# Optimization experiments

Hardware: AMD Instinct MI355X
Metric: run time of the kernel (lower is better)

The kernel has to match this reference:

```python
import jax, jax.numpy as jnp
import numpy as np

B, C, HH, WW = 8, 512, 32, 32
HEADS, GROUPS, EPS = 8, 32, 1e-5


def setup_inputs() -> dict:
    key = jax.random.key(0)
    k0, k1, k2 = jax.random.split(key, 3)
    x = jax.random.normal(k0, (B, C, HH, WW), jnp.float32)
    gamma = jnp.ones((C,), jnp.float32)
    beta = jnp.zeros((C,), jnp.float32)
    # 1x1 convs modeled as (out, in) matrices; fan-in scaling keeps logits sane
    w_qkv = jax.random.normal(k1, (3 * C, C), jnp.float32) * (C ** -0.5)
    b_qkv = jnp.zeros((3 * C,), jnp.float32)
    w_proj = jax.random.normal(k2, (C, C), jnp.float32) * (C ** -0.5)
    b_proj = jnp.zeros((C,), jnp.float32)
    return {"x": x, "gamma": gamma, "beta": beta, "w_qkv": w_qkv,
            "b_qkv": b_qkv, "w_proj": w_proj, "b_proj": b_proj}


def reference(x, gamma, beta, w_qkv, b_qkv, w_proj, b_proj):
    b, c, h, w = x.shape
    S = h * w
    xr = x.reshape(b, c, S)
    # GroupNorm(32, C) over (channels_in_group, spatial)
    xg = xr.reshape(b, GROUPS, c // GROUPS, S)
    mu = xg.mean(axis=(2, 3), keepdims=True)
    var = xg.var(axis=(2, 3), keepdims=True)
    xn = ((xg - mu) * jax.lax.rsqrt(var + EPS)).reshape(b, c, S)
    xn = xn * gamma[None, :, None] + beta[None, :, None]
    # qkv 1x1 conv: (B, 3C, S)
    qkv = jnp.einsum('oc,bcs->bos', w_qkv, xn) + b_qkv[None, :, None]
    D = c // HEADS
    qkv = qkv.reshape(b, 3, HEADS, D, S)  # channel layout: (three, H, D)
    q = jnp.transpose(qkv[:, 0], (0, 1, 3, 2))  # (B, H, S, D)
    k = jnp.transpose(qkv[:, 1], (0, 1, 3, 2))
    v = jnp.transpose(qkv[:, 2], (0, 1, 3, 2))
    scale = 1.0 / float(np.sqrt(np.sqrt(D)))
    logits = jnp.einsum('bhtd,bhsd->bhts', q * scale, k * scale)  # (B,H,S,S)
    logits = logits - jnp.max(logits, axis=-1, keepdims=True)
    probs = jax.nn.softmax(logits, axis=-1)  # dropout p=0 (default)
    attn = jnp.einsum('bhts,bhsd->bhtd', probs, v)  # (B,H,S,D)
    hout = jnp.transpose(attn, (0, 1, 3, 2)).reshape(b, c, S)  # (B, H*D=C, S)
    hout = jnp.einsum('oc,bcs->bos', w_proj, hout) + b_proj[None, :, None]
    return (hout + xr).reshape(b, c, h, w)
```

## Files before the change

### kernel.cpp

```cpp
#include <hip/hip_runtime.h>
#include <hip/hip_bf16.h>

typedef __hip_bfloat16 bf16;
typedef unsigned short u16;
typedef __attribute__((ext_vector_type(8))) short bf16x8;
typedef __attribute__((ext_vector_type(16))) float f32x16;

static constexpr int Bn = 8;
static constexpr int C = 512;
static constexpr int S = 1024;
static constexpr int NH = 8;
static constexpr int HD = 64;
static constexpr int CPG = 16;
#define EPSV 1e-5f
#define QSCALE 0.18033688011112042f

__device__ __forceinline__ u16 f2bf(float f) {
    bf16 h = __float2bfloat16(f);
    return *reinterpret_cast<u16*>(&h);
}
__device__ __forceinline__ unsigned pack_bf2(float a, float b) {
    __hip_bfloat162 h = __float22bfloat162_rn(make_float2(a, b));
    return *reinterpret_cast<unsigned*>(&h);
}

__device__ __forceinline__ void plswap32(unsigned a, unsigned b, unsigned& x, unsigned& y) {
    typedef __attribute__((ext_vector_type(2))) int v2i;
    v2i r = __builtin_amdgcn_permlane32_swap((int)a, (int)b, false, false);
    x = (unsigned)r[0];
    y = (unsigned)r[1];
}

__device__ __forceinline__ void async_copy16(const void* g, void* l) {
    __builtin_amdgcn_global_load_lds(
        (const __attribute__((address_space(1))) void*)g,
        (__attribute__((address_space(3))) void*)l, 16, 0, 0);
}

__global__ __launch_bounds__(256) void prep(const float* __restrict__ x,
                                            const float* __restrict__ wqkv,
                                            const float* __restrict__ wproj,
                                            const float* __restrict__ gamma,
                                            const float* __restrict__ beta,
                                            u16* __restrict__ wbf,
                                            u16* __restrict__ xnt) {
    const int tid = threadIdx.x;
    __shared__ float xs[CPG * S];
    if (blockIdx.x < 256) {
        const int bg = blockIdx.x;
        const int b = bg >> 5, g = bg & 31;
        const size_t base = (size_t)bg * CPG * S;
        const int N = CPG * S;
        float sum = 0.f, sq = 0.f;
        for (int i = tid * 4; i < N; i += 1024) {
            float4 v = *reinterpret_cast<const float4*>(&x[base + i]);
            sum += v.x + v.y + v.z + v.w;
            sq += v.x * v.x + v.y * v.y + v.z * v.z + v.w * v.w;
            *reinterpret_cast<float4*>(&xs[i]) = v;
        }
#pragma unroll
        for (int off = 32; off > 0; off >>= 1) {
            sum += __shfl_down(sum, off, 64);
            sq  += __shfl_down(sq,  off, 64);
        }
        __shared__ float s0[4], s1[4];
        __shared__ float sgb[32];
        __shared__ float smu, srstd;
        if ((tid & 63) == 0) { s0[tid >> 6] = sum; s1[tid >> 6] = sq; }
        if (tid < 16) {
            sgb[tid] = gamma[g * CPG + tid];
            sgb[16 + tid] = beta[g * CPG + tid];
        }
        __syncthreads();
        if (tid == 0) {
            float a  = s0[0] + s0[1] + s0[2] + s0[3];
            float b2 = s1[0] + s1[1] + s1[2] + s1[3];
            float mu = a / (float)N;
            float var = fmaxf(b2 / (float)N - mu * mu, 0.f);
            smu = mu;
            srstd = rsqrtf(var + EPSV);
        }
        __syncthreads();
        const float mu = smu, rstd = srstd;
#pragma unroll
        for (int it = 0; it < 8; ++it) {
            int idx = it * 256 + tid;
            int s = idx >> 1, jh = idx & 1;
            u16 t8[8];
#pragma unroll
            for (int j = 0; j < 8; ++j) {
                int c = jh * 8 + j;
                float v = (xs[c * S + s] - mu) * rstd;
                t8[j] = f2bf(v * sgb[c] + sgb[16 + c]);
            }
            *reinterpret_cast<uint4*>(&xnt[(size_t)(b * S + s) * C + g * CPG + jh * 8]) =
                *reinterpret_cast<uint4*>(t8);
        }
    } else {
        int idx = (blockIdx.x - 256) * 1024 + tid * 4;
        float4 v;
        float sc = 1.f;
        if (idx < 1536 * 512) {
            v = *reinterpret_cast<const float4*>(&wqkv[idx]);
            if (idx < 512 * 512) sc = QSCALE;
        } else {
            v = *reinterpret_cast<const float4*>(&wproj[idx - 1536 * 512]);
        }
        u16 t[4] = {f2bf(v.x * sc), f2bf(v.y * sc), f2bf(v.z * sc), f2bf(v.w * sc)};
        *reinterpret_cast<uint2*>(&wbf[idx]) = *reinterpret_cast<uint2*>(t);
    }
}

__global__ __launch_bounds__(256) void qkv_gemm(const u16* __restrict__ Wb,
                                                const u16* __restrict__ Xt,
                                                const float* __restrict__ bias,
                                                u16* __restrict__ qkvT,
                                                u16* __restrict__ qkvV) {
    const int K = 512;
    const int b = blockIdx.z, o0 = blockIdx.y * 128, s0 = blockIdx.x * 128;
    const int tid = threadIdx.x;
    const int lane = tid & 63, w = tid >> 6;
    const int l31 = lane & 31, half = lane >> 5;
    const int wr = w >> 1, wc = w & 1;
    __shared__ u16 As[128 * 64];
    __shared__ u16 Bs[128 * 64];
    f32x16 acc[2][2] = {};
    const u16* Xb = Xt + (size_t)(b * S + s0) * K;
    for (int k0 = 0; k0 < K; k0 += 64) {
#pragma unroll
        for (int i = 0; i < 4; ++i) {
            int ci = w * 4 + i;
            int r = ci * 8 + (lane >> 3);
            int c = (lane & 7) ^ (r & 7);
            async_copy16(&Wb[(size_t)(o0 + r) * K + k0 + c * 8], &As[ci * 512]);
            async_copy16(&Xb[(size_t)r * K + k0 + c * 8], &Bs[ci * 512]);
        }
        __syncthreads();
#pragma unroll
        for (int kk = 0; kk < 4; ++kk) {
            int c8 = kk * 2 + half;
            bf16x8 af[2], bfr[2];
#pragma unroll
            for (int mt = 0; mt < 2; ++mt) {
                int R = wr * 64 + mt * 32 + l31;
                af[mt] = *reinterpret_cast<const bf16x8*>(
                    &As[R * 64 + ((c8 ^ (R & 7)) << 3)]);
            }
#pragma unroll
            for (int nt = 0; nt < 2; ++nt) {
                int R = wc * 64 + nt * 32 + l31;
                bfr[nt] = *reinterpret_cast<const bf16x8*>(
                    &Bs[R * 64 + ((c8 ^ (R & 7)) << 3)]);
            }
#pragma unroll
            for (int mt = 0; mt < 2; ++mt)
#pragma unroll
                for (int nt = 0; nt < 2; ++nt)
                    acc[mt][nt] = __builtin_amdgcn_mfma_f32_32x32x16_bf16(
                        af[mt], bfr[nt], acc[mt][nt], 0, 0, 0);
        }
        __syncthreads();
    }
    if (o0 < 1024) {
        float bsc = (o0 < 512) ? QSCALE : 1.f;
#pragma unroll
        for (int mt = 0; mt < 2; ++mt) {
#pragma unroll
            for (int g = 0; g < 4; ++g) {
                int o_b = o0 + wr * 64 + mt * 32 + g * 8 + half * 4;
                float4 bz = *reinterpret_cast<const float4*>(&bias[o_b]);
#pragma unroll
                for (int nt = 0; nt < 2; ++nt) {
                    int s = s0 + wc * 64 + nt * 32 + l31;
                    uint2 pk;
                    pk.x = pack_bf2(acc[mt][nt][g * 4 + 0] + bz.x * bsc,
                                    acc[mt][nt][g * 4 + 1] + bz.y * bsc);
                    pk.y = pack_bf2(acc[mt][nt][g * 4 + 2] + bz.z * bsc,
                                    acc[mt][nt][g * 4 + 3] + bz.w * bsc);
                    *reinterpret_cast<uint2*>(&qkvT[(size_t)(b * S + s) * 1024 + o_b]) = pk;
                }
            }
        }
    } else {
#pragma unroll
        for (int mt = 0; mt < 2; ++mt) {
#pragma unroll
            for (int g = 0; g < 4; ++g) {
                int o_b = o0 - 1024 + wr * 64 + mt * 32 + g * 8 + half * 4;
                float4 bz = *reinterpret_cast<const float4*>(&bias[1024 + o_b]);
                float bza[4] = {bz.x, bz.y, bz.z, bz.w};
#pragma unroll
                for (int nt = 0; nt < 2; ++nt) {
                    int s = s0 + wc * 64 + nt * 32 + l31;
#pragma unroll
                    for (int r = 0; r < 4; ++r)
                        qkvV[(size_t)(b * 512 + o_b + r) * S + s] =
                            f2bf(acc[mt][nt][g * 4 + r] + bza[r]);
                }
            }
        }
    }
}

__global__ __launch_bounds__(256) void proj_gemm(const u16* __restrict__ Wb,
                                                 const u16* __restrict__ Xt,
                                                 const float* __restrict__ bias,
                                                 const float* __restrict__ resid,
                                                 float* __restrict__ Yf) {
    const int K = 512;
    const int b = blockIdx.z, o0 = blockIdx.y * 64, s0 = blockIdx.x * 128;
    const int tid = threadIdx.x;
    const int lane = tid & 63, w = tid >> 6;
    const int l31 = lane & 31, half = lane >> 5;
    const int wr = w >> 1, wc = w & 1;
    __shared__ u16 As[64 * 64];
    __shared__ u16 Bs[128 * 64];
    f32x16 acc[2] = {};
    const u16* Xb = Xt + (size_t)(b * S + s0) * K;
    for (int k0 = 0; k0 < K; k0 += 64) {
#pragma unroll
        for (int i = 0; i < 2; ++i) {
            int ci = w * 2 + i;
            int r = ci * 8 + (lane >> 3);
            int c = (lane & 7) ^ (r & 7);
            async_copy16(&Wb[(size_t)(o0 + r) * K + k0 + c * 8], &As[ci * 512]);
        }
#pragma unroll
        for (int i = 0; i < 4; ++i) {
            int ci = w * 4 + i;
            int r = ci * 8 + (lane >> 3);
            int c = (lane & 7) ^ (r & 7);
            async_copy16(&Xb[(size_t)r * K + k0 + c * 8], &Bs[ci * 512]);
        }
        __syncthreads();
#pragma unroll
        for (int kk = 0; kk < 4; ++kk) {
            int c8 = kk * 2 + half;
            int Ra = wr * 32 + l31;
            bf16x8 af = *reinterpret_cast<const bf16x8*>(
                &As[Ra * 64 + ((c8 ^ (Ra & 7)) << 3)]);
#pragma unroll
            for (int nt = 0; nt < 2; ++nt) {
                int R = wc * 64 + nt * 32 + l31;
                bf16x8 bfr = *reinterpret_cast<const bf16x8*>(
                    &Bs[R * 64 + ((c8 ^ (R & 7)) << 3)]);
                acc[nt] = __builtin_amdgcn_mfma_f32_32x32x16_bf16(
                    af, bfr, acc[nt], 0, 0, 0);
            }
        }
        __syncthreads();
    }
#pragma unroll
    for (int g = 0; g < 4; ++g) {
        int o_b = o0 + wr * 32 + g * 8 + half * 4;
        float4 bz = *reinterpret_cast<const float4*>(&bias[o_b]);
        float bza[4] = {bz.x, bz.y, bz.z, bz.w};
#pragma unroll
        for (int nt = 0; nt < 2; ++nt) {
            int s = s0 + wc * 64 + nt * 32 + l31;
#pragma unroll
            for (int r = 0; r < 4; ++r) {
                size_t idx = (size_t)(b * C + o_b + r) * S + s;
                Yf[idx] = acc[nt][g * 4 + r] + bza[r] + resid[idx];
            }
        }
    }
}

__global__ __launch_bounds__(256) void attn_mfma(const u16* __restrict__ qkvT,
                                                 const u16* __restrict__ qkvV,
                                                 u16* __restrict__ houtt) {
    const int b = blockIdx.x >> 3, h = blockIdx.x & 7, q0 = blockIdx.y * 128;
    const int tid = threadIdx.x;
    const int lane = tid & 63, w = tid >> 6;
    const int l31 = lane & 31, half = lane >> 5;
    __shared__ u16 ks[2][64 * 64];
    __shared__ u16 vs[2][64 * 64];

    const u16* qrow = qkvT + (size_t)(b * S + q0 + w * 32 + l31) * 1024 + h * HD;
    const u16* krow = qkvT + (size_t)b * S * 1024 + 512 + h * HD;
    const u16* vrow = qkvV + (size_t)(b * 512 + h * HD) * S;

    bf16x8 qfrag[4];
#pragma unroll
    for (int kk = 0; kk < 4; ++kk)
        qfrag[kk] = *reinterpret_cast<const bf16x8*>(&qrow[kk * 16 + half * 8]);

#pragma unroll
    for (int i = 0; i < 2; ++i) {
        int ci = w * 2 + i;
        int r = ci * 8 + (lane >> 3);
        int c = (lane & 7) ^ (r & 7);
        async_copy16(&krow[(size_t)r * 1024 + c * 8], &ks[0][ci * 512]);
        async_copy16(&vrow[(size_t)r * S + c * 8], &vs[0][ci * 512]);
    }
    __syncthreads();

    f32x16 o_acc[2] = {};
    float l_i = 0.f;

    for (int t = 0; t < 16; ++t) {
        const int cur = t & 1, nxt = cur ^ 1;
        if (t < 15) {
            int kt = (t + 1) * 64;
#pragma unroll
            for (int i = 0; i < 2; ++i) {
                int ci = w * 2 + i;
                int r = ci * 8 + (lane >> 3);
                int c = (lane & 7) ^ (r & 7);
                async_copy16(&krow[(size_t)(kt + r) * 1024 + c * 8], &ks[nxt][ci * 512]);
                async_copy16(&vrow[(size_t)r * S + kt + c * 8], &vs[nxt][ci * 512]);
            }
        }
        f32x16 s_acc[2] = {};
        __builtin_amdgcn_s_setprio(1);
#pragma unroll
        for (int mt = 0; mt < 2; ++mt) {
            int r = mt * 32 + l31;
#pragma unroll
            for (int kk = 0; kk < 4; ++kk) {
                int c8 = kk * 2 + half;
                bf16x8 kf = *reinterpret_cast<const bf16x8*>(
                    &ks[cur][r * 64 + ((c8 ^ (r & 7)) << 3)]);
                s_acc[mt] = __builtin_amdgcn_mfma_f32_32x32x16_bf16(
                    kf, qfrag[kk], s_acc[mt], 0, 0, 0);
            }
        }
        __builtin_amdgcn_s_setprio(0);
        float rsp0 = 0.f, rsp1 = 0.f, rsp2 = 0.f, rsp3 = 0.f;
#pragma unroll
        for (int mt = 0; mt < 2; ++mt)
#pragma unroll
            for (int g = 0; g < 4; ++g) {
                float p0 = __builtin_amdgcn_exp2f(s_acc[mt][g * 4 + 0]);
                float p1 = __builtin_amdgcn_exp2f(s_acc[mt][g * 4 + 1]);
                float p2 = __builtin_amdgcn_exp2f(s_acc[mt][g * 4 + 2]);
                float p3 = __builtin_amdgcn_exp2f(s_acc[mt][g * 4 + 3]);
                s_acc[mt][g * 4 + 0] = p0;
                s_acc[mt][g * 4 + 1] = p1;
                s_acc[mt][g * 4 + 2] = p2;
                s_acc[mt][g * 4 + 3] = p3;
                rsp0 += p0; rsp1 += p1; rsp2 += p2; rsp3 += p3;
            }
        l_i += (rsp0 + rsp1) + (rsp2 + rsp3);
        bf16x8 pf[4];
#pragma unroll
        for (int mt = 0; mt < 2; ++mt)
#pragma unroll
            for (int gp = 0; gp < 2; ++gp) {
                unsigned a_lo = pack_bf2(s_acc[mt][gp * 8 + 0], s_acc[mt][gp * 8 + 1]);
                unsigned a_hi = pack_bf2(s_acc[mt][gp * 8 + 2], s_acc[mt][gp * 8 + 3]);
                unsigned b_lo = pack_bf2(s_acc[mt][gp * 8 + 4], s_acc[mt][gp * 8 + 5]);
                unsigned b_hi = pack_bf2(s_acc[mt][gp * 8 + 6], s_acc[mt][gp * 8 + 7]);
                unsigned u0, u1, u2, u3;
                plswap32(a_lo, b_lo, u0, u2);
                plswap32(a_hi, b_hi, u1, u3);
                union { unsigned u[4]; bf16x8 v; } wv;
                wv.u[0] = u0; wv.u[1] = u1; wv.u[2] = u2; wv.u[3] = u3;
                pf[mt * 2 + gp] = wv.v;
            }
        __builtin_amdgcn_s_setprio(1);
#pragma unroll
        for (int nt = 0; nt < 2; ++nt) {
            int rv = nt * 32 + l31;
#pragma unroll
            for (int kk = 0; kk < 4; ++kk) {
                int c8 = kk * 2 + half;
                bf16x8 vf = *reinterpret_cast<const bf16x8*>(
                    &vs[cur][rv * 64 + ((c8 ^ (rv & 7)) << 3)]);
                o_acc[nt] = __builtin_amdgcn_mfma_f32_32x32x16_bf16(
                    vf, pf[kk], o_acc[nt], 0, 0, 0);
            }
        }
        __builtin_amdgcn_s_setprio(0);
        __syncthreads();
    }
    l_i += __shfl_xor(l_i, 32, 64);
    float inv = 1.f / l_i;
    u16* orow = houtt + (size_t)(b * S + q0 + w * 32 + l31) * 512 + h * HD;
#pragma unroll
    for (int nt = 0; nt < 2; ++nt)
#pragma unroll
        for (int g = 0; g < 4; ++g) {
            uint2 pk;
            pk.x = pack_bf2(o_acc[nt][g * 4 + 0] * inv, o_acc[nt][g * 4 + 1] * inv);
            pk.y = pack_bf2(o_acc[nt][g * 4 + 2] * inv, o_acc[nt][g * 4 + 3] * inv);
            *reinterpret_cast<uint2*>(&orow[nt * 32 + g * 8 + half * 4]) = pk;
        }
}

extern "C" void kernel_launch(void* const* d_in, const int* in_sizes, int n_in,
                              void* d_out, int out_size, void* d_ws, size_t ws_size,
                              hipStream_t stream) {
    const float* x      = (const float*)d_in[0];
    const float* gamma  = (const float*)d_in[1];
    const float* beta   = (const float*)d_in[2];
    const float* w_qkv  = (const float*)d_in[3];
    const float* b_qkv  = (const float*)d_in[4];
    const float* w_proj = (const float*)d_in[5];
    const float* b_proj = (const float*)d_in[6];
    float* out = (float*)d_out;

    char* ws = (char*)d_ws;
    u16* wbf   = (u16*)ws;
    u16* xnt   = (u16*)(ws + 2097152);
    u16* qkvT  = (u16*)(ws + 2097152 + 8388608);
    u16* qkvV  = (u16*)(ws + 2097152 + 8388608 + 16777216);
    u16* houtt = xnt;

    prep<<<1280, 256, 0, stream>>>(x, w_qkv, w_proj, gamma, beta, wbf, xnt);
    qkv_gemm<<<dim3(8, 12, Bn), 256, 0, stream>>>(wbf, xnt, b_qkv, qkvT, qkvV);
    attn_mfma<<<dim3(Bn * NH, S / 128), 256, 0, stream>>>(qkvT, qkvV, houtt);
    proj_gemm<<<dim3(8, 8, Bn), 256, 0, stream>>>(
        wbf + 1536 * 512, houtt, b_proj, x, out);
}
```

Measured before the change: 152.9 us.

## Process 128-key tiles per iteration in attention kernel with launch bounds

The attention kernel now loads and processes 128 keys per loop iteration instead of 64, using two 64-key sub-tiles in the double-buffered shared memory, which halves the number of barriers and loop iterations. It also adds a min-blocks-per-CU hint of 2 to launch bounds. The cost is doubled LDS usage (64 KB per block) and more live registers for the score and probability fragments, which could limit occupancy or cause spills.

Result: no change. 150.3 us, median of 2 (-1.7%).

```diff
diff --git a/kernel.cpp b/kernel.cpp
--- a/kernel.cpp
+++ b/kernel.cpp
@@ -267,15 +267,15 @@
     }
 }
 
-__global__ __launch_bounds__(256) void attn_mfma(const u16* __restrict__ qkvT,
-                                                 const u16* __restrict__ qkvV,
-                                                 u16* __restrict__ houtt) {
+__global__ __launch_bounds__(256, 2) void attn_mfma(const u16* __restrict__ qkvT,
+                                                    const u16* __restrict__ qkvV,
+                                                    u16* __restrict__ houtt) {
     const int b = blockIdx.x >> 3, h = blockIdx.x & 7, q0 = blockIdx.y * 128;
     const int tid = threadIdx.x;
     const int lane = tid & 63, w = tid >> 6;
     const int l31 = lane & 31, half = lane >> 5;
-    __shared__ u16 ks[2][64 * 64];
-    __shared__ u16 vs[2][64 * 64];
+    __shared__ u16 ks[2][2][64 * 64];
+    __shared__ u16 vs[2][2][64 * 64];
 
     const u16* qrow = qkvT + (size_t)(b * S + q0 + w * 32 + l31) * 1024 + h * HD;
     const u16* krow = qkvT + (size_t)b * S * 1024 + 512 + h * HD;
@@ -286,88 +286,100 @@
     for (int kk = 0; kk < 4; ++kk)
         qfrag[kk] = *reinterpret_cast<const bf16x8*>(&qrow[kk * 16 + half * 8]);
 
-#pragma unroll
-    for (int i = 0; i < 2; ++i) {
-        int ci = w * 2 + i;
-        int r = ci * 8 + (lane >> 3);
-        int c = (lane & 7) ^ (r & 7);
-        async_copy16(&krow[(size_t)r * 1024 + c * 8], &ks[0][ci * 512]);
-        async_copy16(&vrow[(size_t)r * S + c * 8], &vs[0][ci * 512]);
-    }
+    const int r8 = lane >> 3;
+    const int cc = lane & 7;
+
+#pragma unroll
+    for (int kh = 0; kh < 2; ++kh)
+#pragma unroll
+        for (int i = 0; i < 2; ++i) {
+            int ci = w * 2 + i;
+            int r = ci * 8 + r8;
+            int c = cc ^ (r & 7);
+            async_copy16(&krow[(size_t)(kh * 64 + r) * 1024 + c * 8], &ks[0][kh][ci * 512]);
+            async_copy16(&vrow[(size_t)r * S + kh * 64 + c * 8], &vs[0][kh][ci * 512]);
+        }
     __syncthreads();
 
     f32x16 o_acc[2] = {};
     float l_i = 0.f;
 
-    for (int t = 0; t < 16; ++t) {
+    for (int t = 0; t < 8; ++t) {
         const int cur = t & 1, nxt = cur ^ 1;
-        if (t < 15) {
-            int kt = (t + 1) * 64;
-#pragma unroll
-            for (int i = 0; i < 2; ++i) {
-                int ci = w * 2 + i;
-                int r = ci * 8 + (lane >> 3);
-                int c = (lane & 7) ^ (r & 7);
-                async_copy16(&krow[(size_t)(kt + r) * 1024 + c * 8], &ks[nxt][ci * 512]);
-                async_copy16(&vrow[(size_t)r * S + kt + c * 8], &vs[nxt][ci * 512]);
-            }
-        }
-        f32x16 s_acc[2] = {};
+        if (t < 7) {
+            int kt = (t + 1) * 128;
+#pragma unroll
+            for (int kh = 0; kh < 2; ++kh)
+#pragma unroll
+                for (int i = 0; i < 2; ++i) {
+                    int ci = w * 2 + i;
+                    int r = ci * 8 + r8;
+                    int c = cc ^ (r & 7);
+                    async_copy16(&krow[(size_t)(kt + kh * 64 + r) * 1024 + c * 8],
+                                 &ks[nxt][kh][ci * 512]);
+                    async_copy16(&vrow[(size_t)r * S + kt + kh * 64 + c * 8],
+                                 &vs[nxt][kh][ci * 512]);
+                }
+        }
+        f32x16 s_acc[4] = {};
         __builtin_amdgcn_s_setprio(1);
 #pragma unroll
-        for (int mt = 0; mt < 2; ++mt) {
-            int r = mt * 32 + l31;
+        for (int a = 0; a < 4; ++a) {
+            int r = (a & 1) * 32 + l31;
+            const u16* kbase = &ks[cur][a >> 1][0];
 #pragma unroll
             for (int kk = 0; kk < 4; ++kk) {
                 int c8 = kk * 2 + half;
                 bf16x8 kf = *reinterpret_cast<const bf16x8*>(
-                    &ks[cur][r * 64 + ((c8 ^ (r & 7)) << 3)]);
-                s_acc[mt] = __builtin_amdgcn_mfma_f32_32x32x16_bf16(
-                    kf, qfrag[kk], s_acc[mt], 0, 0, 0);
+                    &kbase[r * 64 + ((c8 ^ (r & 7)) << 3)]);
+                s_acc[a] = __builtin_amdgcn_mfma_f32_32x32x16_bf16(
+                    kf, qfrag[kk], s_acc[a], 0, 0, 0);
             }
         }
         __builtin_amdgcn_s_setprio(0);
         float rsp0 = 0.f, rsp1 = 0.f, rsp2 = 0.f, rsp3 = 0.f;
 #pragma unroll
-        for (int mt = 0; mt < 2; ++mt)
+        for (int a = 0; a < 4; ++a)
 #pragma unroll
             for (int g = 0; g < 4; ++g) {
-                float p0 = __builtin_amdgcn_exp2f(s_acc[mt][g * 4 + 0]);
-                float p1 = __builtin_amdgcn_exp2f(s_acc[mt][g * 4 + 1]);
-                float p2 = __builtin_amdgcn_exp2f(s_acc[mt][g * 4 + 2]);
-                float p3 = __builtin_amdgcn_exp2f(s_acc[mt][g * 4 + 3]);
-                s_acc[mt][g * 4 + 0] = p0;
-                s_acc[mt][g * 4 + 1] = p1;
-                s_acc[mt][g * 4 + 2] = p2;
-                s_acc[mt][g * 4 + 3] = p3;
+                float p0 = __builtin_amdgcn_exp2f(s_acc[a][g * 4 + 0]);
+                float p1 = __builtin_amdgcn_exp2f(s_acc[a][g * 4 + 1]);
+                float p2 = __builtin_amdgcn_exp2f(s_acc[a][g * 4 + 2]);
+                float p3 = __builtin_amdgcn_exp2f(s_acc[a][g * 4 + 3]);
+                s_acc[a][g * 4 + 0] = p0;
+                s_acc[a][g * 4 + 1] = p1;
+                s_acc[a][g * 4 + 2] = p2;
+                s_acc[a][g * 4 + 3] = p3;
                 rsp0 += p0; rsp1 += p1; rsp2 += p2; rsp3 += p3;
             }
         l_i += (rsp0 + rsp1) + (rsp2 + rsp3);
-        bf16x8 pf[4];
-#pragma unroll
-        for (int mt = 0; mt < 2; ++mt)
+        bf16x8 pf[8];
+#pragma unroll
+        for (int a = 0; a < 4; ++a)
 #pragma unroll
             for (int gp = 0; gp < 2; ++gp) {
-                unsigned a_lo = pack_bf2(s_acc[mt][gp * 8 + 0], s_acc[mt][gp * 8 + 1]);
-                unsigned a_hi = pack_bf2(s_acc[mt][gp * 8 + 2], s_acc[mt][gp * 8 + 3]);
-                unsigned b_lo = pack_bf2(s_acc[mt][gp * 8 + 4], s_acc[mt][gp * 8 + 5]);
-                unsigned b_hi = pack_bf2(s_acc[mt][gp * 8 + 6], s_acc[mt][gp * 8 + 7]);
+                unsigned a_lo = pack_bf2(s_acc[a][gp * 8 + 0], s_acc[a][gp * 8 + 1]);
+                unsigned a_hi = pack_bf2(s_acc[a][gp * 8 + 2], s_acc[a][gp * 8 + 3]);
+                unsigned b_lo = pack_bf2(s_acc[a][gp * 8 + 4], s_acc[a][gp * 8 + 5]);
+                unsigned b_hi = pack_bf2(s_acc[a][gp * 8 + 6], s_acc[a][gp * 8 + 7]);
                 unsigned u0, u1, u2, u3;
                 plswap32(a_lo, b_lo, u0, u2);
                 plswap32(a_hi, b_hi, u1, u3);
                 union { unsigned u[4]; bf16x8 v; } wv;
                 wv.u[0] = u0; wv.u[1] = u1; wv.u[2] = u2; wv.u[3] = u3;
-                pf[mt * 2 + gp] = wv.v;
+                pf[a * 2 + gp] = wv.v;
             }
         __builtin_amdgcn_s_setprio(1);
 #pragma unroll
         for (int nt = 0; nt < 2; ++nt) {
             int rv = nt * 32 + l31;
 #pragma unroll
-            for (int kk = 0; kk < 4; ++kk) {
+            for (int kk = 0; kk < 8; ++kk) {
                 int c8 = kk * 2 + half;
+                const u16* vbase = &vs[cur][c8 >> 3][0];
+                int c8l = c8 & 7;
                 bf16x8 vf = *reinterpret_cast<const bf16x8*>(
-                    &vs[cur][rv * 64 + ((c8 ^ (rv & 7)) << 3)]);
+                    &vbase[rv * 64 + ((c8l ^ (rv & 7)) << 3)]);
                 o_acc[nt] = __builtin_amdgcn_mfma_f32_32x32x16_bf16(
                     vf, pf[kk], o_acc[nt], 0, 0, 0);
             }
```

## Process two query tiles per wave in attention to reuse K/V fragments

Applied to the files above, without the earlier changes.

The attention kernel now runs 2 waves per block instead of 4, with each wave handling 64 query rows (two 32-row tiles) instead of 32. Each K and V fragment read from shared memory feeds MFMAs for both query tiles, halving LDS reads per MFMA. Each wave also issues twice the async copies per tile. The cost is higher register pressure from the doubled accumulators and fragments, and fewer waves per block to hide latency at barriers.

New measurement: 159.8 us. 4.5% more time.

```diff
diff --git a/kernel.cpp b/kernel.cpp
--- a/kernel.cpp
+++ b/kernel.cpp
@@ -267,7 +267,7 @@
     }
 }
 
-__global__ __launch_bounds__(256) void attn_mfma(const u16* __restrict__ qkvT,
+__global__ __launch_bounds__(128) void attn_mfma(const u16* __restrict__ qkvT,
                                                  const u16* __restrict__ qkvV,
                                                  u16* __restrict__ houtt) {
     const int b = blockIdx.x >> 3, h = blockIdx.x & 7, q0 = blockIdx.y * 128;
@@ -277,116 +277,142 @@
     __shared__ u16 ks[2][64 * 64];
     __shared__ u16 vs[2][64 * 64];
 
-    const u16* qrow = qkvT + (size_t)(b * S + q0 + w * 32 + l31) * 1024 + h * HD;
     const u16* krow = qkvT + (size_t)b * S * 1024 + 512 + h * HD;
     const u16* vrow = qkvV + (size_t)(b * 512 + h * HD) * S;
 
-    bf16x8 qfrag[4];
-#pragma unroll
-    for (int kk = 0; kk < 4; ++kk)
-        qfrag[kk] = *reinterpret_cast<const bf16x8*>(&qrow[kk * 16 + half * 8]);
-
-#pragma unroll
-    for (int i = 0; i < 2; ++i) {
-        int ci = w * 2 + i;
-        int r = ci * 8 + (lane >> 3);
-        int c = (lane & 7) ^ (r & 7);
+    bf16x8 qfrag[2][4];
+#pragma unroll
+    for (int qt = 0; qt < 2; ++qt) {
+        const u16* qrow =
+            qkvT + (size_t)(b * S + q0 + w * 64 + qt * 32 + l31) * 1024 + h * HD;
+#pragma unroll
+        for (int kk = 0; kk < 4; ++kk)
+            qfrag[qt][kk] = *reinterpret_cast<const bf16x8*>(&qrow[kk * 16 + half * 8]);
+    }
+
+    const int r8 = lane >> 3;
+    const int cc = lane & 7;
+
+#pragma unroll
+    for (int i = 0; i < 4; ++i) {
+        int ci = w * 4 + i;
+        int r = ci * 8 + r8;
+        int c = cc ^ (r & 7);
         async_copy16(&krow[(size_t)r * 1024 + c * 8], &ks[0][ci * 512]);
         async_copy16(&vrow[(size_t)r * S + c * 8], &vs[0][ci * 512]);
     }
     __syncthreads();
 
-    f32x16 o_acc[2] = {};
-    float l_i = 0.f;
+    f32x16 o_acc[2][2] = {};
+    float l_i[2] = {0.f, 0.f};
 
     for (int t = 0; t < 16; ++t) {
         const int cur = t & 1, nxt = cur ^ 1;
         if (t < 15) {
             int kt = (t + 1) * 64;
 #pragma unroll
-            for (int i = 0; i < 2; ++i) {
-                int ci = w * 2 + i;
-                int r = ci * 8 + (lane >> 3);
-                int c = (lane & 7) ^ (r & 7);
+            for (int i = 0; i < 4; ++i) {
+                int ci = w * 4 + i;
+                int r = ci * 8 + r8;
+                int c = cc ^ (r & 7);
                 async_copy16(&krow[(size_t)(kt + r) * 1024 + c * 8], &ks[nxt][ci * 512]);
                 async_copy16(&vrow[(size_t)r * S + kt + c * 8], &vs[nxt][ci * 512]);
             }
         }
-        f32x16 s_acc[2] = {};
+        f32x16 s_acc[2][2] = {};
         __builtin_amdgcn_s_setprio(1);
 #pragma unroll
         for (int mt = 0; mt < 2; ++mt) {
             int r = mt * 32 + l31;
-#pragma unroll
-            for (int kk = 0; kk < 4; ++kk) {
-                int c8 = kk * 2 + half;
-                bf16x8 kf = *reinterpret_cast<const bf16x8*>(
-                    &ks[cur][r * 64 + ((c8 ^ (r & 7)) << 3)]);
-                s_acc[mt] = __builtin_amdgcn_mfma_f32_32x32x16_bf16(
-                    kf, qfrag[kk], s_acc[mt], 0, 0, 0);
-            }
+            bf16x8 kf[4];
+#pragma unroll
+            for (int kk = 0; kk < 4; ++kk)
+                kf[kk] = *reinterpret_cast<const bf16x8*>(
+                    &ks[cur][r * 64 + (((kk * 2 + half) ^ (r & 7)) << 3)]);
+#pragma unroll
+            for (int qt = 0; qt < 2; ++qt)
+#pragma unroll
+                for (int kk = 0; kk < 4; ++kk)
+                    s_acc[qt][mt] = __builtin_amdgcn_mfma_f32_32x32x16_bf16(
+                        kf[kk], qfrag[qt][kk], s_acc[qt][mt], 0, 0, 0);
         }
         __builtin_amdgcn_s_setprio(0);
-        float rsp0 = 0.f, rsp1 = 0.f, rsp2 = 0.f, rsp3 = 0.f;
-#pragma unroll
-        for (int mt = 0; mt < 2; ++mt)
-#pragma unroll
-            for (int g = 0; g < 4; ++g) {
-                float p0 = __builtin_amdgcn_exp2f(s_acc[mt][g * 4 + 0]);
-                float p1 = __builtin_amdgcn_exp2f(s_acc[mt][g * 4 + 1]);
-                float p2 = __builtin_amdgcn_exp2f(s_acc[mt][g * 4 + 2]);
-                float p3 = __builtin_amdgcn_exp2f(s_acc[mt][g * 4 + 3]);
-                s_acc[mt][g * 4 + 0] = p0;
-                s_acc[mt][g * 4 + 1] = p1;
-                s_acc[mt][g * 4 + 2] = p2;
-                s_acc[mt][g * 4 + 3] = p3;
-                rsp0 += p0; rsp1 += p1; rsp2 += p2; rsp3 += p3;
-            }
-        l_i += (rsp0 + rsp1) + (rsp2 + rsp3);
-        bf16x8 pf[4];
-#pragma unroll
-        for (int mt = 0; mt < 2; ++mt)
-#pragma unroll
-            for (int gp = 0; gp < 2; ++gp) {
-                unsigned a_lo = pack_bf2(s_acc[mt][gp * 8 + 0], s_acc[mt][gp * 8 + 1]);
-                unsigned a_hi = pack_bf2(s_acc[mt][gp * 8 + 2], s_acc[mt][gp * 8 + 3]);
-                unsigned b_lo = pack_bf2(s_acc[mt][gp * 8 + 4], s_acc[mt][gp * 8 + 5]);
-                unsigned b_hi = pack_bf2(s_acc[mt][gp * 8 + 6], s_acc[mt][gp * 8 + 7]);
-                unsigned u0, u1, u2, u3;
-                plswap32(a_lo, b_lo, u0, u2);
-                plswap32(a_hi, b_hi, u1, u3);
-                union { unsigned u[4]; bf16x8 v; } wv;
-                wv.u[0] = u0; wv.u[1] = u1; wv.u[2] = u2; wv.u[3] = u3;
-                pf[mt * 2 + gp] = wv.v;
-            }
+        bf16x8 pf[2][4];
+#pragma unroll
+        for (int qt = 0; qt < 2; ++qt) {
+            float rsp0 = 0.f, rsp1 = 0.f, rsp2 = 0.f, rsp3 = 0.f;
+#pragma unroll
+            for (int mt = 0; mt < 2; ++mt)
+#pragma unroll
+                for (int g = 0; g < 4; ++g) {
+                    float p0 = __builtin_amdgcn_exp2f(s_acc[qt][mt][g * 4 + 0]);
+                    float p1 = __builtin_amdgcn_exp2f(s_acc[qt][mt][g * 4 + 1]);
+                    float p2 = __builtin_amdgcn_exp2f(s_acc[qt][mt][g * 4 + 2]);
+                    float p3 = __builtin_amdgcn_exp2f(s_acc[qt][mt][g * 4 + 3]);
+                    s_acc[qt][mt][g * 4 + 0] = p0;
+                    s_acc[qt][mt][g * 4 + 1] = p1;
+                    s_acc[qt][mt][g * 4 + 2] = p2;
+                    s_acc[qt][mt][g * 4 + 3] = p3;
+                    rsp0 += p0; rsp1 += p1; rsp2 += p2; rsp3 += p3;
+                }
+            l_i[qt] += (rsp0 + rsp1) + (rsp2 + rsp3);
+#pragma unroll
+            for (int mt = 0; mt < 2; ++mt)
+#pragma unroll
+                for (int gp = 0; gp < 2; ++gp) {
+                    unsigned a_lo = pack_bf2(s_acc[qt][mt][gp * 8 + 0],
+                                             s_acc[qt][mt][gp * 8 + 1]);
+                    unsigned a_hi = pack_bf2(s_acc[qt][mt][gp * 8 + 2],
+                                             s_acc[qt][mt][gp * 8 + 3]);
+                    unsigned b_lo = pack_bf2(s_acc[qt][mt][gp * 8 + 4],
+                                             s_acc[qt][mt][gp * 8 + 5]);
+                    unsigned b_hi = pack_bf2(s_acc[qt][mt][gp * 8 + 6],
+                                             s_acc[qt][mt][gp * 8 + 7]);
+                    unsigned u0, u1, u2, u3;
+                    plswap32(a_lo, b_lo, u0, u2);
+                    plswap32(a_hi, b_hi, u1, u3);
+                    union { unsigned u[4]; bf16x8 v; } wv;
+                    wv.u[0] = u0; wv.u[1] = u1; wv.u[2] = u2; wv.u[3] = u3;
+                    pf[qt][mt * 2 + gp] = wv.v;
+                }
+        }
         __builtin_amdgcn_s_setprio(1);
 #pragma unroll
         for (int nt = 0; nt < 2; ++nt) {
             int rv = nt * 32 + l31;
-#pragma unroll
-            for (int kk = 0; kk < 4; ++kk) {
-                int c8 = kk * 2 + half;
-                bf16x8 vf = *reinterpret_cast<const bf16x8*>(
-                    &vs[cur][rv * 64 + ((c8 ^ (rv & 7)) << 3)]);
-                o_acc[nt] = __builtin_amdgcn_mfma_f32_32x32x16_bf16(
-                    vf, pf[kk], o_acc[nt], 0, 0, 0);
-            }
+            bf16x8 vf[4];
+#pragma unroll
+            for (int kk = 0; kk < 4; ++kk)
+                vf[kk] = *reinterpret_cast<const bf16x8*>(
+                    &vs[cur][rv * 64 + (((kk * 2 + half) ^ (rv & 7)) << 3)]);
+#pragma unroll
+            for (int qt = 0; qt < 2; ++qt)
+#pragma unroll
+                for (int kk = 0; kk < 4; ++kk)
+                    o_acc[qt][nt] = __builtin_amdgcn_mfma_f32_32x32x16_bf16(
+                        vf[kk], pf[qt][kk], o_acc[qt][nt], 0, 0, 0);
         }
         __builtin_amdgcn_s_setprio(0);
         __syncthreads();
     }
-    l_i += __shfl_xor(l_i, 32, 64);
-    float inv = 1.f / l_i;
-    u16* orow = houtt + (size_t)(b * S + q0 + w * 32 + l31) * 512 + h * HD;
-#pragma unroll
-    for (int nt = 0; nt < 2; ++nt)
-#pragma unroll
-        for (int g = 0; g < 4; ++g) {
-            uint2 pk;
-            pk.x = pack_bf2(o_acc[nt][g * 4 + 0] * inv, o_acc[nt][g * 4 + 1] * inv);
-            pk.y = pack_bf2(o_acc[nt][g * 4 + 2] * inv, o_acc[nt][g * 4 + 3] * inv);
-            *reinterpret_cast<uint2*>(&orow[nt * 32 + g * 8 + half * 4]) = pk;
-        }
+#pragma unroll
+    for (int qt = 0; qt < 2; ++qt) {
+        float li = l_i[qt] + __shfl_xor(l_i[qt], 32, 64);
+        float inv = 1.f / li;
+        u16* orow =
+            houtt + (size_t)(b * S + q0 + w * 64 + qt * 32 + l31) * 512 + h * HD;
+#pragma unroll
+        for (int nt = 0; nt < 2; ++nt)
+#pragma unroll
+            for (int g = 0; g < 4; ++g) {
+                uint2 pk;
+                pk.x = pack_bf2(o_acc[qt][nt][g * 4 + 0] * inv,
+                                o_acc[qt][nt][g * 4 + 1] * inv);
+                pk.y = pack_bf2(o_acc[qt][nt][g * 4 + 2] * inv,
+                                o_acc[qt][nt][g * 4 + 3] * inv);
+                *reinterpret_cast<uint2*>(&orow[nt * 32 + g * 8 + half * 4]) = pk;
+            }
+    }
 }
 
 extern "C" void kernel_launch(void* const* d_in, const int* in_sizes, int n_in,
@@ -410,7 +436,7 @@
 
     prep<<<1280, 256, 0, stream>>>(x, w_qkv, w_proj, gamma, beta, wbf, xnt);
     qkv_gemm<<<dim3(8, 12, Bn), 256, 0, stream>>>(wbf, xnt, b_qkv, qkvT, qkvV);
-    attn_mfma<<<dim3(Bn * NH, S / 128), 256, 0, stream>>>(qkvT, qkvV, houtt);
+    attn_mfma<<<dim3(Bn * NH, S / 128), 128, 0, stream>>>(qkvT, qkvV, houtt);
     proj_gemm<<<dim3(8, 8, Bn), 256, 0, stream>>>(
         wbf + 1536 * 512, houtt, b_proj, x, out);
 }
```
